# Optimization experiments

Measured on AMD Instinct MI355X. Metric: run time of the kernel, lower is better.

## Reference

```python
import jax, jax.numpy as jnp
import numpy as np

D_MODEL, D_K, D_V = 1024, 64, 64
B, S = 2, 4096
NEG = 1e9


def setup_inputs() -> dict:
    key = jax.random.key(0)
    ks = jax.random.split(key, 10)
    Q = jax.random.normal(ks[0], (B, S, D_MODEL), dtype=jnp.float32)
    K = jax.random.normal(ks[1], (B, S, D_MODEL), dtype=jnp.float32)
    V = jax.random.normal(ks[2], (B, S, D_MODEL), dtype=jnp.float32)
    mask = jax.random.randint(ks[3], (B, S, S), 0, 2, dtype=jnp.int32)
    sc = 1.0 / np.sqrt(D_MODEL)
    Wq = jax.random.normal(ks[4], (D_K, D_MODEL), dtype=jnp.float32) * sc
    bq = jnp.zeros((D_K,), dtype=jnp.float32)
    Wk = jax.random.normal(ks[5], (D_K, D_MODEL), dtype=jnp.float32) * sc
    bk = jnp.zeros((D_K,), dtype=jnp.float32)
    Wv = jax.random.normal(ks[6], (D_V, D_MODEL), dtype=jnp.float32) * sc
    bv = jnp.zeros((D_V,), dtype=jnp.float32)
    return {"Q": Q, "K": K, "V": V, "mask": mask,
            "Wq": Wq, "bq": bq, "Wk": Wk, "bk": bk, "Wv": Wv, "bv": bv}


def reference(Q, K, V, mask, Wq, bq, Wk, bk, Wv, bv):
    # Linear projections: q,k -> [B,S,d_k], v -> [B,S,d_v]
    q = jnp.einsum('bsm,km->bsk', Q, Wq) + bq
    k = jnp.einsum('bsm,km->bsk', K, Wk) + bk
    v = jnp.einsum('bsm,vm->bsv', V, Wv) + bv
    # Scaled dot-product scores [B,S,S]
    x = jnp.einsum('bqk,bsk->bqs', q, k) / jnp.sqrt(jnp.float32(D_K))
    m = mask.astype(x.dtype)
    x = x * m - NEG * (1.0 - m)
    x = jax.nn.softmax(x, axis=2)
    y = jnp.einsum('bqs,bsv->bqv', x, v)
    return y
```

## Files before the change

### kernel.cpp

```cpp
#include <hip/hip_runtime.h>

typedef unsigned short u16;
typedef unsigned long long u64;
typedef __bf16 bf16x8 __attribute__((ext_vector_type(8)));
typedef float f32x4 __attribute__((ext_vector_type(4)));

#define MFMA16(a, b, c) __builtin_amdgcn_mfma_f32_16x16x32_bf16((a), (b), (c), 0, 0, 0)

__device__ __forceinline__ bf16x8 ld8(const u16* p) {
    return *reinterpret_cast<const bf16x8*>(p);
}

__device__ __forceinline__ unsigned pk2(float a, float b) {
    unsigned short ua = __builtin_bit_cast(unsigned short, (__bf16)a);
    unsigned short ub = __builtin_bit_cast(unsigned short, (__bf16)b);
    return (unsigned)ua | ((unsigned)ub << 16);
}

__device__ __forceinline__ bf16x8 cvt8(float4 a, float4 b) {
    bf16x8 r;
    r[0] = (__bf16)a.x; r[1] = (__bf16)a.y; r[2] = (__bf16)a.z; r[3] = (__bf16)a.w;
    r[4] = (__bf16)b.x; r[5] = (__bf16)b.y; r[6] = (__bf16)b.z; r[7] = (__bf16)b.w;
    return r;
}

__global__ __launch_bounds__(256) void packcvt_kernel(
    const int* __restrict__ mask, u64* __restrict__ bits,
    const float* __restrict__ Wq, const float* __restrict__ Wk,
    const float* __restrict__ Wv, u16* __restrict__ wb)
{
    if (blockIdx.x >= 2048) {
        const int t = (blockIdx.x - 2048) * 256 + threadIdx.x;
        const int mat = t >> 13;
        const int idx = (t & 8191) * 8;
        const float* src = (mat == 0) ? Wq : (mat == 1) ? Wk : Wv;
        float4 a = *(const float4*)(src + idx);
        float4 b = *(const float4*)(src + idx + 4);
        uint4 o;
        o.x = pk2(a.x, a.y); o.y = pk2(a.z, a.w);
        o.z = pk2(b.x, b.y); o.w = pk2(b.z, b.w);
        *reinterpret_cast<uint4*>(wb + (size_t)mat * 65536 + idx) = o;
        return;
    }

    const int lane = threadIdx.x & 63, w = threadIdx.x >> 6;
    const int row = blockIdx.x * 4 + w;
    const int* mp = mask + (size_t)row * 4096 + lane * 4;
    u64* op = bits + (size_t)row * 64;

    int4 h0[8], h1[8];
    #pragma unroll
    for (int j = 0; j < 8; ++j) h0[j] = *(const int4*)(mp + j * 256);
    #pragma unroll
    for (int j = 0; j < 8; ++j) h1[j] = *(const int4*)(mp + 2048 + j * 256);

    u64 mine0 = 0, mine1 = 0;
    #pragma unroll
    for (int j = 0; j < 8; ++j) {
        const u64 b0 = __ballot(h0[j].x != 0);
        const u64 b1 = __ballot(h0[j].y != 0);
        const u64 b2 = __ballot(h0[j].z != 0);
        const u64 b3 = __ballot(h0[j].w != 0);
        if (lane == j * 4 + 0) mine0 = b0;
        if (lane == j * 4 + 1) mine0 = b1;
        if (lane == j * 4 + 2) mine0 = b2;
        if (lane == j * 4 + 3) mine0 = b3;
        const u64 c0 = __ballot(h1[j].x != 0);
        const u64 c1 = __ballot(h1[j].y != 0);
        const u64 c2 = __ballot(h1[j].z != 0);
        const u64 c3 = __ballot(h1[j].w != 0);
        if (lane == j * 4 + 0) mine1 = c0;
        if (lane == j * 4 + 1) mine1 = c1;
        if (lane == j * 4 + 2) mine1 = c2;
        if (lane == j * 4 + 3) mine1 = c3;
    }
    if (lane < 32) { op[lane] = mine0; op[32 + lane] = mine1; }
}

__global__ __launch_bounds__(256, 1) void proj_kernel(
    const float* __restrict__ Q, const float* __restrict__ K, const float* __restrict__ V,
    const float* __restrict__ bq, const float* __restrict__ bk, const float* __restrict__ bv,
    const u16* __restrict__ wb, u16* __restrict__ qb, u16* __restrict__ kb,
    u16* __restrict__ vtb)
{
    const int mat  = blockIdx.x >> 7;
    const int tile = blockIdx.x & 127;
    const int lane = threadIdx.x & 63;
    const int w    = threadIdx.x >> 6;
    const int c = lane & 15, g = lane >> 4;

    const float* X = (mat == 0) ? Q : (mat == 1) ? K : V;
    const u16*   W = wb + (size_t)mat * 65536;

    const int rw = tile * 64 + w * 16;
    const float* xp = X + (size_t)(rw + c) * 1024 + g * 8;
    const u16*   wp = W + (size_t)c * 1024 + g * 8;

    f32x4 acc[4] = {};

    float4 A[8], B[8];
    #pragma unroll
    for (int j = 0; j < 8; ++j) {
        A[j] = *(const float4*)(xp + j * 32);
        B[j] = *(const float4*)(xp + j * 32 + 4);
    }

    #pragma unroll 1
    for (int kt = 0; kt < 4; ++kt) {
        const int base  = kt * 8;
        const int nbase = (kt < 3) ? base + 8 : base;
        #pragma unroll
        for (int j = 0; j < 8; ++j) {
            const bf16x8 a = cvt8(A[j], B[j]);
            A[j] = *(const float4*)(xp + (nbase + j) * 32);
            B[j] = *(const float4*)(xp + (nbase + j) * 32 + 4);
            const u16* wk = wp + (base + j) * 32;
            if (mat < 2) {
                #pragma unroll
                for (int t = 0; t < 4; ++t)
                    acc[t] = MFMA16(a, ld8(wk + t * 16384), acc[t]);
            } else {
                #pragma unroll
                for (int t = 0; t < 4; ++t)
                    acc[t] = MFMA16(ld8(wk + t * 16384), a, acc[t]);
            }
        }
    }

    if (mat < 2) {
        const float* bias = (mat == 0) ? bq : bk;
        u16* dst = (mat == 0) ? qb : kb;
        #pragma unroll
        for (int t = 0; t < 4; ++t) {
            const float bz = bias[t * 16 + c];
            #pragma unroll
            for (int r = 0; r < 4; ++r) {
                const int row = rw + g * 4 + r;
                dst[(size_t)row * 64 + t * 16 + c] =
                    __builtin_bit_cast(u16, (__bf16)(acc[t][r] + bz));
            }
        }
    } else {
        const int sg = rw + c;
        const int bidx = sg >> 12, sin = sg & 4095;
        #pragma unroll
        for (int t = 0; t < 4; ++t) {
            #pragma unroll
            for (int r = 0; r < 4; ++r) {
                const int dv = t * 16 + g * 4 + r;
                vtb[(size_t)(bidx * 64 + dv) * 4096 + sin] =
                    __builtin_bit_cast(u16, (__bf16)(acc[t][r] + bv[dv]));
            }
        }
    }
}

__global__ __launch_bounds__(256) void attn_kernel(
    const u64* __restrict__ bits, const u16* __restrict__ qb,
    const u16* __restrict__ kb, const u16* __restrict__ vtb,
    float* __restrict__ pacc, float* __restrict__ pm, float* __restrict__ pl)
{
    __shared__ uint2 plds[4][128];
    const int lane = threadIdx.x & 63, w = threadIdx.x >> 6;
    const int c = lane & 15, g = lane >> 4;
    const int gw    = blockIdx.x * 4 + w;
    const int strip = gw >> 3;
    const int chunk = gw & 7;
    const int b     = strip >> 8;
    const int q0    = (strip & 255) * 16;
    const int sBase = chunk * 512;
    const float SSC = 0.18033688011112042f;

    const u16* qrow = qb + (size_t)((b << 12) + q0 + c) * 64 + g * 8;
    const bf16x8 qf0 = ld8(qrow);
    const bf16x8 qf1 = ld8(qrow + 32);

    const u16* kfp = kb  + (((size_t)b << 12) + sBase + c) * 64 + g * 8;
    const u16* vfp = vtb + (size_t)(b * 64 + c) * 4096 + sBase + g * 8;

    const u64* bp = bits + (size_t)((b << 12) + q0 + c) * 64 + chunk * 8;
    const u64 Wd0 = bp[0], Wd1 = bp[1], Wd2 = bp[2], Wd3 = bp[3];
    const u64 Wd4 = bp[4], Wd5 = bp[5], Wd6 = bp[6], Wd7 = bp[7];

    f32x4 acc0 = {}, acc1 = {}, acc2 = {}, acc3 = {};
    const f32x4 zf = {};
    float m_run = -__builtin_inff(), l_run = 0.f;

    bf16x8 k00 = ld8(kfp),            k01 = ld8(kfp + 32);
    bf16x8 k10 = ld8(kfp + 16 * 64),  k11 = ld8(kfp + 16 * 64 + 32);

    #pragma unroll
    for (int half = 0; half < 2; ++half) {
        const u64 Wr0 = half ? Wd4 : Wd0;
        const u64 Wr1 = half ? Wd5 : Wd1;
        const u64 Wr2 = half ? Wd6 : Wd2;
        const u64 Wr3 = half ? Wd7 : Wd3;
        #pragma unroll 1
        for (int it2 = 0; it2 < 8; ++it2) {
            const int it = half * 8 + it2;
            const int s0 = sBase + it * 32;

            const u16* vp = vfp + it * 32;
            const bf16x8 v0 = ld8(vp);
            const bf16x8 v1 = ld8(vp + 16 * 4096);
            const bf16x8 v2 = ld8(vp + 32 * 4096);
            const bf16x8 v3 = ld8(vp + 48 * 4096);

            f32x4 d0 = MFMA16(k00, qf0, zf);
            d0 = MFMA16(k01, qf1, d0);
            f32x4 d1 = MFMA16(k10, qf0, zf);
            d1 = MFMA16(k11, qf1, d1);

            const int no = (it < 15) ? (it + 1) * 2048 : it * 2048;
            k00 = ld8(kfp + no);            k01 = ld8(kfp + no + 32);
            k10 = ld8(kfp + no + 16 * 64);  k11 = ld8(kfp + no + 16 * 64 + 32);

            const int sh = it2 * 8 + g;
            const unsigned t0 = (unsigned)(Wr0 >> sh);
            const unsigned t1 = (unsigned)(Wr1 >> sh);
            const unsigned t2 = (unsigned)(Wr2 >> sh);
            const unsigned t3 = (unsigned)(Wr3 >> sh);

            const float x0 = (t0 & 1u)  ? d0[0] * SSC : -1e9f;
            const float x1 = (t1 & 1u)  ? d0[1] * SSC : -1e9f;
            const float x2 = (t2 & 1u)  ? d0[2] * SSC : -1e9f;
            const float x3 = (t3 & 1u)  ? d0[3] * SSC : -1e9f;
            const float x4 = (t0 & 16u) ? d1[0] * SSC : -1e9f;
            const float x5 = (t1 & 16u) ? d1[1] * SSC : -1e9f;
            const float x6 = (t2 & 16u) ? d1[2] * SSC : -1e9f;
            const float x7 = (t3 & 16u) ? d1[3] * SSC : -1e9f;

            float tm = fmaxf(fmaxf(fmaxf(x0, x1), fmaxf(x2, x3)),
                             fmaxf(fmaxf(x4, x5), fmaxf(x6, x7)));
            tm = fmaxf(tm, __shfl_xor(tm, 16));
            tm = fmaxf(tm, __shfl_xor(tm, 32));
            const float m_new = fmaxf(m_run, tm);
            const float f = exp2f(m_run - m_new);

            const float p0 = exp2f(x0 - m_new), p1 = exp2f(x1 - m_new);
            const float p2 = exp2f(x2 - m_new), p3 = exp2f(x3 - m_new);
            const float p4 = exp2f(x4 - m_new), p5 = exp2f(x5 - m_new);
            const float p6 = exp2f(x6 - m_new), p7 = exp2f(x7 - m_new);
            float rs = ((p0 + p1) + (p2 + p3)) + ((p4 + p5) + (p6 + p7));
            rs += __shfl_xor(rs, 16);
            rs += __shfl_xor(rs, 32);
            l_run = l_run * f + rs;
            m_run = m_new;

            plds[w][c * 8 + ( g      ^ (c & 7))] = make_uint2(pk2(p0, p1), pk2(p2, p3));
            plds[w][c * 8 + ((g + 4) ^ (c & 7))] = make_uint2(pk2(p4, p5), pk2(p6, p7));

            if (__any(f < 1.0f)) {
                const float f0 = __shfl(f, g * 4 + 0);
                const float f1 = __shfl(f, g * 4 + 1);
                const float f2 = __shfl(f, g * 4 + 2);
                const float f3 = __shfl(f, g * 4 + 3);
                acc0[0] *= f0; acc0[1] *= f1; acc0[2] *= f2; acc0[3] *= f3;
                acc1[0] *= f0; acc1[1] *= f1; acc1[2] *= f2; acc1[3] *= f3;
                acc2[0] *= f0; acc2[1] *= f1; acc2[2] *= f2; acc2[3] *= f3;
                acc3[0] *= f0; acc3[1] *= f1; acc3[2] *= f2; acc3[3] *= f3;
            }

            union { uint2 u[2]; bf16x8 v; } pa;
            pa.u[0] = plds[w][c * 8 + ((2 * g    ) ^ (c & 7))];
            pa.u[1] = plds[w][c * 8 + ((2 * g + 1) ^ (c & 7))];

            acc0 = MFMA16(pa.v, v0, acc0);
            acc1 = MFMA16(pa.v, v1, acc1);
            acc2 = MFMA16(pa.v, v2, acc2);
            acc3 = MFMA16(pa.v, v3, acc3);
        }
    }

    const size_t pidx = (size_t)(strip * 8 + chunk) * 16;
    #pragma unroll
    for (int r = 0; r < 4; ++r) {
        const size_t row = pidx + g * 4 + r;
        pacc[row * 64 +  0 + c] = acc0[r];
        pacc[row * 64 + 16 + c] = acc1[r];
        pacc[row * 64 + 32 + c] = acc2[r];
        pacc[row * 64 + 48 + c] = acc3[r];
    }
    if (lane < 16) {
        pm[pidx + c] = m_run;
        pl[pidx + c] = l_run;
    }
}

__global__ __launch_bounds__(256) void comb_kernel(
    const float* __restrict__ pacc, const float* __restrict__ pm,
    const float* __restrict__ pl, float* __restrict__ out)
{
    const int t = blockIdx.x * 256 + threadIdx.x;
    const int r = t >> 6, dv = t & 63;
    const int strip = r >> 4, qi = r & 15;
    const int base = strip * 128 + qi;
    float mv[8];
    float M = -__builtin_inff();
    #pragma unroll
    for (int cc = 0; cc < 8; ++cc) { mv[cc] = pm[base + cc * 16]; M = fmaxf(M, mv[cc]); }
    float num = 0.f, den = 0.f;
    #pragma unroll
    for (int cc = 0; cc < 8; ++cc) {
        const float wgt = exp2f(mv[cc] - M);
        num += wgt * pacc[(size_t)(base + cc * 16) * 64 + dv];
        den += wgt * pl[base + cc * 16];
    }
    out[t] = num / den;
}

extern "C" void kernel_launch(void* const* d_in, const int* in_sizes, int n_in,
                              void* d_out, int out_size, void* d_ws, size_t ws_size,
                              hipStream_t stream)
{
    const float* Q    = (const float*)d_in[0];
    const float* K    = (const float*)d_in[1];
    const float* V    = (const float*)d_in[2];
    const int*   mask = (const int*)d_in[3];
    const float* Wq   = (const float*)d_in[4];
    const float* bq   = (const float*)d_in[5];
    const float* Wk   = (const float*)d_in[6];
    const float* bk   = (const float*)d_in[7];
    const float* Wv   = (const float*)d_in[8];
    const float* bv   = (const float*)d_in[9];
    float* out = (float*)d_out;

    char* ws = (char*)d_ws;
    u16*   wb   = (u16*)(ws);
    u16*   qb   = (u16*)(ws + 393216);
    u16*   kb   = (u16*)(ws + 393216 + 1048576);
    u16*   vtb  = (u16*)(ws + 393216 + 2097152);
    u64*   bits = (u64*)(ws + 4194304);
    float* pm   = (float*)(ws + 8388608);
    float* pl   = (float*)(ws + 8388608 + 262144);
    float* pacc = (float*)(ws + 8388608 + 524288);

    packcvt_kernel<<<2144, 256, 0, stream>>>(mask, bits, Wq, Wk, Wv, wb);
    proj_kernel<<<384, 256, 0, stream>>>(Q, K, V, bq, bk, bv, wb, qb, kb, vtb);
    attn_kernel<<<1024, 256, 0, stream>>>(bits, qb, kb, vtb, pacc, pm, pl);
    comb_kernel<<<2048, 256, 0, stream>>>(pacc, pm, pl, out);
}
```

Baseline: 145.5 us.

## Fuse mask bit-packing into projection kernel with async LDS-staged loads

Splits weight conversion into its own small kernel and merges the mask-to-bitmask packing with the Q/K/V projection into one launch. Projection blocks and mask blocks now run concurrently, so the bandwidth-bound mask read can overlap the MFMA-bound projection. Both paths stage global data through LDS with global_load_lds in a three-slot ring, with explicit vmcnt waits and an XOR swizzle on the activation tiles. The projection blocks lose the `(256, 1)` launch bound, and the hand-written waitcnt schedule is fragile if the compiler reorders loads.

```diff
diff --git a/kernel.cpp b/kernel.cpp
--- a/kernel.cpp
+++ b/kernel.cpp
@@ -6,6 +6,13 @@
 typedef float f32x4 __attribute__((ext_vector_type(4)));
 
 #define MFMA16(a, b, c) __builtin_amdgcn_mfma_f32_16x16x32_bf16((a), (b), (c), 0, 0, 0)
+#define WAITVM(N) asm volatile("s_waitcnt vmcnt(" #N ")" ::: "memory")
+
+__device__ __forceinline__ void gld16(const void* g, void* l) {
+    __builtin_amdgcn_global_load_lds(
+        (const __attribute__((address_space(1))) void*)g,
+        (__attribute__((address_space(3))) void*)l, 16, 0, 0);
+}
 
 __device__ __forceinline__ bf16x8 ld8(const u16* p) {
     return *reinterpret_cast<const bf16x8*>(p);
@@ -24,107 +31,124 @@
     return r;
 }
 
-__global__ __launch_bounds__(256) void packcvt_kernel(
-    const int* __restrict__ mask, u64* __restrict__ bits,
+__global__ __launch_bounds__(256) void wcvt_kernel(
     const float* __restrict__ Wq, const float* __restrict__ Wk,
     const float* __restrict__ Wv, u16* __restrict__ wb)
 {
-    if (blockIdx.x >= 2048) {
-        const int t = (blockIdx.x - 2048) * 256 + threadIdx.x;
-        const int mat = t >> 13;
-        const int idx = (t & 8191) * 8;
-        const float* src = (mat == 0) ? Wq : (mat == 1) ? Wk : Wv;
-        float4 a = *(const float4*)(src + idx);
-        float4 b = *(const float4*)(src + idx + 4);
-        uint4 o;
-        o.x = pk2(a.x, a.y); o.y = pk2(a.z, a.w);
-        o.z = pk2(b.x, b.y); o.w = pk2(b.z, b.w);
-        *reinterpret_cast<uint4*>(wb + (size_t)mat * 65536 + idx) = o;
-        return;
-    }
-
-    const int lane = threadIdx.x & 63, w = threadIdx.x >> 6;
-    const int row = blockIdx.x * 4 + w;
-    const int* mp = mask + (size_t)row * 4096 + lane * 4;
-    u64* op = bits + (size_t)row * 64;
-
-    int4 h0[8], h1[8];
-    #pragma unroll
-    for (int j = 0; j < 8; ++j) h0[j] = *(const int4*)(mp + j * 256);
-    #pragma unroll
-    for (int j = 0; j < 8; ++j) h1[j] = *(const int4*)(mp + 2048 + j * 256);
-
-    u64 mine0 = 0, mine1 = 0;
-    #pragma unroll
-    for (int j = 0; j < 8; ++j) {
-        const u64 b0 = __ballot(h0[j].x != 0);
-        const u64 b1 = __ballot(h0[j].y != 0);
-        const u64 b2 = __ballot(h0[j].z != 0);
-        const u64 b3 = __ballot(h0[j].w != 0);
-        if (lane == j * 4 + 0) mine0 = b0;
-        if (lane == j * 4 + 1) mine0 = b1;
-        if (lane == j * 4 + 2) mine0 = b2;
-        if (lane == j * 4 + 3) mine0 = b3;
-        const u64 c0 = __ballot(h1[j].x != 0);
-        const u64 c1 = __ballot(h1[j].y != 0);
-        const u64 c2 = __ballot(h1[j].z != 0);
-        const u64 c3 = __ballot(h1[j].w != 0);
-        if (lane == j * 4 + 0) mine1 = c0;
-        if (lane == j * 4 + 1) mine1 = c1;
-        if (lane == j * 4 + 2) mine1 = c2;
-        if (lane == j * 4 + 3) mine1 = c3;
-    }
-    if (lane < 32) { op[lane] = mine0; op[32 + lane] = mine1; }
-}
-
-__global__ __launch_bounds__(256, 1) void proj_kernel(
+    const int t = blockIdx.x * 256 + threadIdx.x;
+    const int mat = t >> 13;
+    const int idx = (t & 8191) * 8;
+    const float* src = (mat == 0) ? Wq : (mat == 1) ? Wk : Wv;
+    float4 a = *(const float4*)(src + idx);
+    float4 b = *(const float4*)(src + idx + 4);
+    uint4 o;
+    o.x = pk2(a.x, a.y); o.y = pk2(a.z, a.w);
+    o.z = pk2(b.x, b.y); o.w = pk2(b.z, b.w);
+    *reinterpret_cast<uint4*>(wb + (size_t)mat * 65536 + idx) = o;
+}
+
+__global__ __launch_bounds__(256) void fused_kernel(
     const float* __restrict__ Q, const float* __restrict__ K, const float* __restrict__ V,
     const float* __restrict__ bq, const float* __restrict__ bk, const float* __restrict__ bv,
-    const u16* __restrict__ wb, u16* __restrict__ qb, u16* __restrict__ kb,
-    u16* __restrict__ vtb)
-{
+    const u16* __restrict__ wb, const int* __restrict__ mask,
+    u16* __restrict__ qb, u16* __restrict__ kb, u16* __restrict__ vtb,
+    u64* __restrict__ bits)
+{
+    __shared__ float ldsf[4][3][512];
+    const int lane = threadIdx.x & 63, w = threadIdx.x >> 6;
+
+    if (blockIdx.x >= 384) {
+        const int gwv = (blockIdx.x - 384) * 4 + w;
+        const int row = gwv >> 1, h = gwv & 1;
+        const int* mp = mask + (size_t)row * 4096 + h * 2048 + lane * 4;
+        int* ldsw = (int*)&ldsf[w][0][0];
+
+        gld16(mp +    0, ldsw +    0);
+        gld16(mp +  256, ldsw +  256);
+        gld16(mp +  512, ldsw +  512);
+        gld16(mp +  768, ldsw +  768);
+
+        u64 mine = 0;
+        #pragma unroll
+        for (int st = 0; st < 4; ++st) {
+            const int slot = st % 3;
+            if (st < 2) {
+                gld16(mp + (st + 2) * 512,       ldsw + ((st + 2) % 3) * 512);
+                gld16(mp + (st + 2) * 512 + 256, ldsw + ((st + 2) % 3) * 512 + 256);
+            }
+            if (st < 2)       { WAITVM(4); }
+            else if (st == 2) { WAITVM(2); }
+            else              { WAITVM(0); }
+            #pragma unroll
+            for (int wdw = 0; wdw < 2; ++wdw) {
+                const int4 m4 = *(const int4*)(ldsw + slot * 512 + wdw * 256 + lane * 4);
+                const u64 b0 = __ballot(m4.x != 0);
+                const u64 b1 = __ballot(m4.y != 0);
+                const u64 b2 = __ballot(m4.z != 0);
+                const u64 b3 = __ballot(m4.w != 0);
+                const int base = (st * 2 + wdw) * 4;
+                if (lane == base + 0) mine = b0;
+                if (lane == base + 1) mine = b1;
+                if (lane == base + 2) mine = b2;
+                if (lane == base + 3) mine = b3;
+            }
+        }
+        if (lane < 32) bits[(size_t)row * 64 + h * 32 + lane] = mine;
+        return;
+    }
+
     const int mat  = blockIdx.x >> 7;
     const int tile = blockIdx.x & 127;
-    const int lane = threadIdx.x & 63;
-    const int w    = threadIdx.x >> 6;
     const int c = lane & 15, g = lane >> 4;
 
     const float* X = (mat == 0) ? Q : (mat == 1) ? K : V;
     const u16*   W = wb + (size_t)mat * 65536;
-
     const int rw = tile * 64 + w * 16;
-    const float* xp = X + (size_t)(rw + c) * 1024 + g * 8;
-    const u16*   wp = W + (size_t)c * 1024 + g * 8;
-
+
+    const int srow = lane >> 3;
+    const int sgr  = (lane & 7) ^ srow;
+    const float* s0p = X + (size_t)(rw + srow) * 1024 + sgr * 4;
+    const float* s1p = s0p + 8 * 1024;
+    float* ldsw = &ldsf[w][0][0];
+
+    const int G1 = c * 8 + ((2 * g)     ^ (c & 7));
+    const int G2 = c * 8 + ((2 * g + 1) ^ (c & 7));
+
+    const u16* wp = W + (size_t)c * 1024 + g * 8;
     f32x4 acc[4] = {};
 
-    float4 A[8], B[8];
-    #pragma unroll
-    for (int j = 0; j < 8; ++j) {
-        A[j] = *(const float4*)(xp + j * 32);
-        B[j] = *(const float4*)(xp + j * 32 + 4);
-    }
-
+    gld16(s0p +  0, ldsw +    0);
+    gld16(s1p +  0, ldsw +  256);
+    gld16(s0p + 32, ldsw +  512);
+    gld16(s1p + 32, ldsw +  768);
+
+    int slot = 0;
     #pragma unroll 1
-    for (int kt = 0; kt < 4; ++kt) {
-        const int base  = kt * 8;
-        const int nbase = (kt < 3) ? base + 8 : base;
-        #pragma unroll
-        for (int j = 0; j < 8; ++j) {
-            const bf16x8 a = cvt8(A[j], B[j]);
-            A[j] = *(const float4*)(xp + (nbase + j) * 32);
-            B[j] = *(const float4*)(xp + (nbase + j) * 32 + 4);
-            const u16* wk = wp + (base + j) * 32;
-            if (mat < 2) {
-                #pragma unroll
-                for (int t = 0; t < 4; ++t)
-                    acc[t] = MFMA16(a, ld8(wk + t * 16384), acc[t]);
-            } else {
-                #pragma unroll
-                for (int t = 0; t < 4; ++t)
-                    acc[t] = MFMA16(ld8(wk + t * 16384), a, acc[t]);
-            }
-        }
+    for (int kk = 0; kk < 32; ++kk) {
+        if (kk < 30) {
+            const int ns = (slot == 0) ? 2 : slot - 1;
+            gld16(s0p + (kk + 2) * 32, ldsw + ns * 512);
+            gld16(s1p + (kk + 2) * 32, ldsw + ns * 512 + 256);
+        }
+        if (kk < 30)       { WAITVM(4); }
+        else if (kk == 30) { WAITVM(2); }
+        else               { WAITVM(0); }
+
+        const float4 xa = *(const float4*)(ldsw + slot * 512 + G1 * 4);
+        const float4 xb = *(const float4*)(ldsw + slot * 512 + G2 * 4);
+        const bf16x8 a = cvt8(xa, xb);
+
+        const u16* wk = wp + kk * 32;
+        if (mat < 2) {
+            #pragma unroll
+            for (int t = 0; t < 4; ++t)
+                acc[t] = MFMA16(a, ld8(wk + t * 16384), acc[t]);
+        } else {
+            #pragma unroll
+            for (int t = 0; t < 4; ++t)
+                acc[t] = MFMA16(ld8(wk + t * 16384), a, acc[t]);
+        }
+        slot = (slot == 2) ? 0 : slot + 1;
     }
 
     if (mat < 2) {
@@ -198,7 +222,6 @@
         #pragma unroll 1
         for (int it2 = 0; it2 < 8; ++it2) {
             const int it = half * 8 + it2;
-            const int s0 = sBase + it * 32;
 
             const u16* vp = vfp + it * 32;
             const bf16x8 v0 = ld8(vp);
@@ -335,8 +358,9 @@
     float* pl   = (float*)(ws + 8388608 + 262144);
     float* pacc = (float*)(ws + 8388608 + 524288);
 
-    packcvt_kernel<<<2144, 256, 0, stream>>>(mask, bits, Wq, Wk, Wv, wb);
-    proj_kernel<<<384, 256, 0, stream>>>(Q, K, V, bq, bk, bv, wb, qb, kb, vtb);
+    wcvt_kernel<<<96, 256, 0, stream>>>(Wq, Wk, Wv, wb);
+    fused_kernel<<<4480, 256, 0, stream>>>(Q, K, V, bq, bk, bv, wb, mask,
+                                           qb, kb, vtb, bits);
     attn_kernel<<<1024, 256, 0, stream>>>(bits, qb, kb, vtb, pacc, pm, pl);
     comb_kernel<<<2048, 256, 0, stream>>>(pacc, pm, pl, out);
 }
```

Measured after the change: 127.1 us. -12.6%, faster.

## Split mask packing into grid-strided kernel and stagger projection K-loop phases

Applied to the files above, without the earlier changes.

The combined pack/convert kernel is split into a small weight-conversion kernel and a separate mask-bit packing kernel. The packing kernel processes 256-int chunks with a grid-strided layout and a 4-deep rolling prefetch, so each wave writes 4 u64 words per chunk rather than buffering 16 loads per row. The projection kernel rotates each wave's K-dimension start by a per-wave phase, which spreads concurrent accesses across different weight and input columns to reduce channel or cache conflicts. It also shortens the prefetch depth from 8 to 4, fully unrolls the loop and drops the occupancy-1 launch bound. The extra launch adds a little overhead, and the reduced prefetch depth may expose more load latency.

```diff
diff --git a/kernel.cpp b/kernel.cpp
--- a/kernel.cpp
+++ b/kernel.cpp
@@ -24,60 +24,54 @@
     return r;
 }
 
-__global__ __launch_bounds__(256) void packcvt_kernel(
-    const int* __restrict__ mask, u64* __restrict__ bits,
+__global__ __launch_bounds__(256) void wcvt_kernel(
     const float* __restrict__ Wq, const float* __restrict__ Wk,
     const float* __restrict__ Wv, u16* __restrict__ wb)
 {
-    if (blockIdx.x >= 2048) {
-        const int t = (blockIdx.x - 2048) * 256 + threadIdx.x;
-        const int mat = t >> 13;
-        const int idx = (t & 8191) * 8;
-        const float* src = (mat == 0) ? Wq : (mat == 1) ? Wk : Wv;
-        float4 a = *(const float4*)(src + idx);
-        float4 b = *(const float4*)(src + idx + 4);
-        uint4 o;
-        o.x = pk2(a.x, a.y); o.y = pk2(a.z, a.w);
-        o.z = pk2(b.x, b.y); o.w = pk2(b.z, b.w);
-        *reinterpret_cast<uint4*>(wb + (size_t)mat * 65536 + idx) = o;
-        return;
-    }
-
-    const int lane = threadIdx.x & 63, w = threadIdx.x >> 6;
-    const int row = blockIdx.x * 4 + w;
-    const int* mp = mask + (size_t)row * 4096 + lane * 4;
-    u64* op = bits + (size_t)row * 64;
-
-    int4 h0[8], h1[8];
-    #pragma unroll
-    for (int j = 0; j < 8; ++j) h0[j] = *(const int4*)(mp + j * 256);
-    #pragma unroll
-    for (int j = 0; j < 8; ++j) h1[j] = *(const int4*)(mp + 2048 + j * 256);
-
-    u64 mine0 = 0, mine1 = 0;
-    #pragma unroll
-    for (int j = 0; j < 8; ++j) {
-        const u64 b0 = __ballot(h0[j].x != 0);
-        const u64 b1 = __ballot(h0[j].y != 0);
-        const u64 b2 = __ballot(h0[j].z != 0);
-        const u64 b3 = __ballot(h0[j].w != 0);
-        if (lane == j * 4 + 0) mine0 = b0;
-        if (lane == j * 4 + 1) mine0 = b1;
-        if (lane == j * 4 + 2) mine0 = b2;
-        if (lane == j * 4 + 3) mine0 = b3;
-        const u64 c0 = __ballot(h1[j].x != 0);
-        const u64 c1 = __ballot(h1[j].y != 0);
-        const u64 c2 = __ballot(h1[j].z != 0);
-        const u64 c3 = __ballot(h1[j].w != 0);
-        if (lane == j * 4 + 0) mine1 = c0;
-        if (lane == j * 4 + 1) mine1 = c1;
-        if (lane == j * 4 + 2) mine1 = c2;
-        if (lane == j * 4 + 3) mine1 = c3;
-    }
-    if (lane < 32) { op[lane] = mine0; op[32 + lane] = mine1; }
-}
-
-__global__ __launch_bounds__(256, 1) void proj_kernel(
+    const int t = blockIdx.x * 256 + threadIdx.x;
+    const int mat = t >> 13;
+    const int idx = (t & 8191) * 8;
+    const float* src = (mat == 0) ? Wq : (mat == 1) ? Wk : Wv;
+    float4 a = *(const float4*)(src + idx);
+    float4 b = *(const float4*)(src + idx + 4);
+    uint4 o;
+    o.x = pk2(a.x, a.y); o.y = pk2(a.z, a.w);
+    o.z = pk2(b.x, b.y); o.w = pk2(b.z, b.w);
+    *reinterpret_cast<uint4*>(wb + (size_t)mat * 65536 + idx) = o;
+}
+
+__global__ __launch_bounds__(256) void pack_kernel(
+    const int* __restrict__ mask, u64* __restrict__ bits)
+{
+    const int lane = threadIdx.x & 63;
+    const int g = (blockIdx.x * 256 + threadIdx.x) >> 6;
+    const int W = gridDim.x * 4;
+
+    int4 h[4];
+    #pragma unroll
+    for (int k = 0; k < 4; ++k)
+        h[k] = *(const int4*)(mask + (size_t)(g + k * W) * 256 + lane * 4);
+
+    #pragma unroll
+    for (int k = 0; k < 16; ++k) {
+        const int4 m4 = h[k & 3];
+        if (k < 12)
+            h[k & 3] = *(const int4*)(mask + (size_t)(g + (k + 4) * W) * 256 + lane * 4);
+
+        const u64 b0 = __ballot(m4.x != 0);
+        const u64 b1 = __ballot(m4.y != 0);
+        const u64 b2 = __ballot(m4.z != 0);
+        const u64 b3 = __ballot(m4.w != 0);
+        u64 myb = b0;
+        if (lane == 1) myb = b1;
+        if (lane == 2) myb = b2;
+        if (lane == 3) myb = b3;
+        const size_t s = (size_t)(g + k * W);
+        if (lane < 4) bits[s * 4 + lane] = myb;
+    }
+}
+
+__global__ __launch_bounds__(256) void proj_kernel(
     const float* __restrict__ Q, const float* __restrict__ K, const float* __restrict__ V,
     const float* __restrict__ bq, const float* __restrict__ bk, const float* __restrict__ bv,
     const u16* __restrict__ wb, u16* __restrict__ qb, u16* __restrict__ kb,
@@ -88,6 +82,7 @@
     const int lane = threadIdx.x & 63;
     const int w    = threadIdx.x >> 6;
     const int c = lane & 15, g = lane >> 4;
+    const int phase = (tile * 4 + w) & 31;
 
     const float* X = (mat == 0) ? Q : (mat == 1) ? K : V;
     const u16*   W = wb + (size_t)mat * 65536;
@@ -98,32 +93,32 @@
 
     f32x4 acc[4] = {};
 
-    float4 A[8], B[8];
-    #pragma unroll
-    for (int j = 0; j < 8; ++j) {
-        A[j] = *(const float4*)(xp + j * 32);
-        B[j] = *(const float4*)(xp + j * 32 + 4);
-    }
-
-    #pragma unroll 1
-    for (int kt = 0; kt < 4; ++kt) {
-        const int base  = kt * 8;
-        const int nbase = (kt < 3) ? base + 8 : base;
-        #pragma unroll
-        for (int j = 0; j < 8; ++j) {
-            const bf16x8 a = cvt8(A[j], B[j]);
-            A[j] = *(const float4*)(xp + (nbase + j) * 32);
-            B[j] = *(const float4*)(xp + (nbase + j) * 32 + 4);
-            const u16* wk = wp + (base + j) * 32;
-            if (mat < 2) {
-                #pragma unroll
-                for (int t = 0; t < 4; ++t)
-                    acc[t] = MFMA16(a, ld8(wk + t * 16384), acc[t]);
-            } else {
-                #pragma unroll
-                for (int t = 0; t < 4; ++t)
-                    acc[t] = MFMA16(ld8(wk + t * 16384), a, acc[t]);
-            }
+    float4 A[4], B[4];
+    #pragma unroll
+    for (int j = 0; j < 4; ++j) {
+        const int kka = (phase + j) & 31;
+        A[j] = *(const float4*)(xp + kka * 32);
+        B[j] = *(const float4*)(xp + kka * 32 + 4);
+    }
+
+    #pragma unroll
+    for (int kk = 0; kk < 32; ++kk) {
+        const int kka = (phase + kk) & 31;
+        const bf16x8 a = cvt8(A[kk & 3], B[kk & 3]);
+        if (kk < 28) {
+            const int kn = (phase + kk + 4) & 31;
+            A[kk & 3] = *(const float4*)(xp + kn * 32);
+            B[kk & 3] = *(const float4*)(xp + kn * 32 + 4);
+        }
+        const u16* wk = wp + kka * 32;
+        if (mat < 2) {
+            #pragma unroll
+            for (int t = 0; t < 4; ++t)
+                acc[t] = MFMA16(a, ld8(wk + t * 16384), acc[t]);
+        } else {
+            #pragma unroll
+            for (int t = 0; t < 4; ++t)
+                acc[t] = MFMA16(ld8(wk + t * 16384), a, acc[t]);
         }
     }
 
@@ -198,7 +193,6 @@
         #pragma unroll 1
         for (int it2 = 0; it2 < 8; ++it2) {
             const int it = half * 8 + it2;
-            const int s0 = sBase + it * 32;
 
             const u16* vp = vfp + it * 32;
             const bf16x8 v0 = ld8(vp);
@@ -335,7 +329,8 @@
     float* pl   = (float*)(ws + 8388608 + 262144);
     float* pacc = (float*)(ws + 8388608 + 524288);
 
-    packcvt_kernel<<<2144, 256, 0, stream>>>(mask, bits, Wq, Wk, Wv, wb);
+    wcvt_kernel<<<96, 256, 0, stream>>>(Wq, Wk, Wv, wb);
+    pack_kernel<<<2048, 256, 0, stream>>>(mask, bits);
     proj_kernel<<<384, 256, 0, stream>>>(Q, K, V, bq, bk, bv, wb, qb, kb, vtb);
     attn_kernel<<<1024, 256, 0, stream>>>(bits, qb, kb, vtb, pacc, pm, pl);
     comb_kernel<<<2048, 256, 0, stream>>>(pacc, pm, pl, out);
```

Measured after the change: 147.8 us. Within noise of the previous version (+1.6%).

## Merge mask bit-packing into projection kernel and use nontemporal streaming loads

Applied to the files above, without the earlier changes.

Splits the weight conversion into its own small kernel and puts the mask bit-packing blocks into the same launch as the Q/K/V projection blocks. Both phases are memory-bound and now run concurrently instead of back-to-back. Mask and activation reads use nontemporal loads to avoid polluting cache. The projection's prefetch depth drops from 8 to 4 and its loop is fully unrolled, which lowers register pressure now that launch_bounds no longer forces one block per SM.

```diff
diff --git a/kernel.cpp b/kernel.cpp
--- a/kernel.cpp
+++ b/kernel.cpp
@@ -4,6 +4,7 @@
 typedef unsigned long long u64;
 typedef __bf16 bf16x8 __attribute__((ext_vector_type(8)));
 typedef float f32x4 __attribute__((ext_vector_type(4)));
+typedef int i32x4 __attribute__((ext_vector_type(4)));
 
 #define MFMA16(a, b, c) __builtin_amdgcn_mfma_f32_16x16x32_bf16((a), (b), (c), 0, 0, 0)
 
@@ -17,76 +18,82 @@
     return (unsigned)ua | ((unsigned)ub << 16);
 }
 
-__device__ __forceinline__ bf16x8 cvt8(float4 a, float4 b) {
+__device__ __forceinline__ bf16x8 cvt8(f32x4 a, f32x4 b) {
     bf16x8 r;
-    r[0] = (__bf16)a.x; r[1] = (__bf16)a.y; r[2] = (__bf16)a.z; r[3] = (__bf16)a.w;
-    r[4] = (__bf16)b.x; r[5] = (__bf16)b.y; r[6] = (__bf16)b.z; r[7] = (__bf16)b.w;
+    r[0] = (__bf16)a[0]; r[1] = (__bf16)a[1]; r[2] = (__bf16)a[2]; r[3] = (__bf16)a[3];
+    r[4] = (__bf16)b[0]; r[5] = (__bf16)b[1]; r[6] = (__bf16)b[2]; r[7] = (__bf16)b[3];
     return r;
 }
 
-__global__ __launch_bounds__(256) void packcvt_kernel(
-    const int* __restrict__ mask, u64* __restrict__ bits,
+__device__ __forceinline__ f32x4 ntf4(const float* p) {
+    return __builtin_nontemporal_load(reinterpret_cast<const f32x4*>(p));
+}
+__device__ __forceinline__ i32x4 nti4(const int* p) {
+    return __builtin_nontemporal_load(reinterpret_cast<const i32x4*>(p));
+}
+
+__global__ __launch_bounds__(256) void wcvt_kernel(
     const float* __restrict__ Wq, const float* __restrict__ Wk,
     const float* __restrict__ Wv, u16* __restrict__ wb)
 {
-    if (blockIdx.x >= 2048) {
-        const int t = (blockIdx.x - 2048) * 256 + threadIdx.x;
-        const int mat = t >> 13;
-        const int idx = (t & 8191) * 8;
-        const float* src = (mat == 0) ? Wq : (mat == 1) ? Wk : Wv;
-        float4 a = *(const float4*)(src + idx);
-        float4 b = *(const float4*)(src + idx + 4);
-        uint4 o;
-        o.x = pk2(a.x, a.y); o.y = pk2(a.z, a.w);
-        o.z = pk2(b.x, b.y); o.w = pk2(b.z, b.w);
-        *reinterpret_cast<uint4*>(wb + (size_t)mat * 65536 + idx) = o;
-        return;
-    }
-
-    const int lane = threadIdx.x & 63, w = threadIdx.x >> 6;
-    const int row = blockIdx.x * 4 + w;
-    const int* mp = mask + (size_t)row * 4096 + lane * 4;
-    u64* op = bits + (size_t)row * 64;
-
-    int4 h0[8], h1[8];
-    #pragma unroll
-    for (int j = 0; j < 8; ++j) h0[j] = *(const int4*)(mp + j * 256);
-    #pragma unroll
-    for (int j = 0; j < 8; ++j) h1[j] = *(const int4*)(mp + 2048 + j * 256);
-
-    u64 mine0 = 0, mine1 = 0;
-    #pragma unroll
-    for (int j = 0; j < 8; ++j) {
-        const u64 b0 = __ballot(h0[j].x != 0);
-        const u64 b1 = __ballot(h0[j].y != 0);
-        const u64 b2 = __ballot(h0[j].z != 0);
-        const u64 b3 = __ballot(h0[j].w != 0);
-        if (lane == j * 4 + 0) mine0 = b0;
-        if (lane == j * 4 + 1) mine0 = b1;
-        if (lane == j * 4 + 2) mine0 = b2;
-        if (lane == j * 4 + 3) mine0 = b3;
-        const u64 c0 = __ballot(h1[j].x != 0);
-        const u64 c1 = __ballot(h1[j].y != 0);
-        const u64 c2 = __ballot(h1[j].z != 0);
-        const u64 c3 = __ballot(h1[j].w != 0);
-        if (lane == j * 4 + 0) mine1 = c0;
-        if (lane == j * 4 + 1) mine1 = c1;
-        if (lane == j * 4 + 2) mine1 = c2;
-        if (lane == j * 4 + 3) mine1 = c3;
-    }
-    if (lane < 32) { op[lane] = mine0; op[32 + lane] = mine1; }
-}
-
-__global__ __launch_bounds__(256, 1) void proj_kernel(
+    const int t = blockIdx.x * 256 + threadIdx.x;
+    const int mat = t >> 13;
+    const int idx = (t & 8191) * 8;
+    const float* src = (mat == 0) ? Wq : (mat == 1) ? Wk : Wv;
+    const f32x4 a = *(const f32x4*)(src + idx);
+    const f32x4 b = *(const f32x4*)(src + idx + 4);
+    uint4 o;
+    o.x = pk2(a[0], a[1]); o.y = pk2(a[2], a[3]);
+    o.z = pk2(b[0], b[1]); o.w = pk2(b[2], b[3]);
+    *reinterpret_cast<uint4*>(wb + (size_t)mat * 65536 + idx) = o;
+}
+
+__global__ __launch_bounds__(256) void fused_kernel(
     const float* __restrict__ Q, const float* __restrict__ K, const float* __restrict__ V,
     const float* __restrict__ bq, const float* __restrict__ bk, const float* __restrict__ bv,
-    const u16* __restrict__ wb, u16* __restrict__ qb, u16* __restrict__ kb,
-    u16* __restrict__ vtb)
-{
+    const u16* __restrict__ wb, const int* __restrict__ mask,
+    u16* __restrict__ qb, u16* __restrict__ kb, u16* __restrict__ vtb,
+    u64* __restrict__ bits)
+{
+    const int lane = threadIdx.x & 63, w = threadIdx.x >> 6;
+
+    if (blockIdx.x >= 384) {
+        const int row = (blockIdx.x - 384) * 4 + w;
+        const int* mp = mask + (size_t)row * 4096 + lane * 4;
+        u64* op = bits + (size_t)row * 64;
+
+        i32x4 h0[8], h1[8];
+        #pragma unroll
+        for (int j = 0; j < 8; ++j) h0[j] = nti4(mp + j * 256);
+        #pragma unroll
+        for (int j = 0; j < 8; ++j) h1[j] = nti4(mp + 2048 + j * 256);
+
+        u64 mine0 = 0, mine1 = 0;
+        #pragma unroll
+        for (int j = 0; j < 8; ++j) {
+            const u64 b0 = __ballot(h0[j][0] != 0);
+            const u64 b1 = __ballot(h0[j][1] != 0);
+            const u64 b2 = __ballot(h0[j][2] != 0);
+            const u64 b3 = __ballot(h0[j][3] != 0);
+            if (lane == j * 4 + 0) mine0 = b0;
+            if (lane == j * 4 + 1) mine0 = b1;
+            if (lane == j * 4 + 2) mine0 = b2;
+            if (lane == j * 4 + 3) mine0 = b3;
+            const u64 c0 = __ballot(h1[j][0] != 0);
+            const u64 c1 = __ballot(h1[j][1] != 0);
+            const u64 c2 = __ballot(h1[j][2] != 0);
+            const u64 c3 = __ballot(h1[j][3] != 0);
+            if (lane == j * 4 + 0) mine1 = c0;
+            if (lane == j * 4 + 1) mine1 = c1;
+            if (lane == j * 4 + 2) mine1 = c2;
+            if (lane == j * 4 + 3) mine1 = c3;
+        }
+        if (lane < 32) { op[lane] = mine0; op[32 + lane] = mine1; }
+        return;
+    }
+
     const int mat  = blockIdx.x >> 7;
     const int tile = blockIdx.x & 127;
-    const int lane = threadIdx.x & 63;
-    const int w    = threadIdx.x >> 6;
     const int c = lane & 15, g = lane >> 4;
 
     const float* X = (mat == 0) ? Q : (mat == 1) ? K : V;
@@ -98,32 +105,29 @@
 
     f32x4 acc[4] = {};
 
-    float4 A[8], B[8];
-    #pragma unroll
-    for (int j = 0; j < 8; ++j) {
-        A[j] = *(const float4*)(xp + j * 32);
-        B[j] = *(const float4*)(xp + j * 32 + 4);
-    }
-
-    #pragma unroll 1
-    for (int kt = 0; kt < 4; ++kt) {
-        const int base  = kt * 8;
-        const int nbase = (kt < 3) ? base + 8 : base;
-        #pragma unroll
-        for (int j = 0; j < 8; ++j) {
-            const bf16x8 a = cvt8(A[j], B[j]);
-            A[j] = *(const float4*)(xp + (nbase + j) * 32);
-            B[j] = *(const float4*)(xp + (nbase + j) * 32 + 4);
-            const u16* wk = wp + (base + j) * 32;
-            if (mat < 2) {
-                #pragma unroll
-                for (int t = 0; t < 4; ++t)
-                    acc[t] = MFMA16(a, ld8(wk + t * 16384), acc[t]);
-            } else {
-                #pragma unroll
-                for (int t = 0; t < 4; ++t)
-                    acc[t] = MFMA16(ld8(wk + t * 16384), a, acc[t]);
-            }
+    f32x4 A[4], B[4];
+    #pragma unroll
+    for (int j = 0; j < 4; ++j) {
+        A[j] = ntf4(xp + j * 32);
+        B[j] = ntf4(xp + j * 32 + 4);
+    }
+
+    #pragma unroll
+    for (int kk = 0; kk < 32; ++kk) {
+        const bf16x8 a = cvt8(A[kk & 3], B[kk & 3]);
+        if (kk < 28) {
+            A[kk & 3] = ntf4(xp + (kk + 4) * 32);
+            B[kk & 3] = ntf4(xp + (kk + 4) * 32 + 4);
+        }
+        const u16* wk = wp + kk * 32;
+        if (mat < 2) {
+            #pragma unroll
+            for (int t = 0; t < 4; ++t)
+                acc[t] = MFMA16(a, ld8(wk + t * 16384), acc[t]);
+        } else {
+            #pragma unroll
+            for (int t = 0; t < 4; ++t)
+                acc[t] = MFMA16(ld8(wk + t * 16384), a, acc[t]);
         }
     }
 
@@ -198,7 +202,6 @@
         #pragma unroll 1
         for (int it2 = 0; it2 < 8; ++it2) {
             const int it = half * 8 + it2;
-            const int s0 = sBase + it * 32;
 
             const u16* vp = vfp + it * 32;
             const bf16x8 v0 = ld8(vp);
@@ -335,8 +338,9 @@
     float* pl   = (float*)(ws + 8388608 + 262144);
     float* pacc = (float*)(ws + 8388608 + 524288);
 
-    packcvt_kernel<<<2144, 256, 0, stream>>>(mask, bits, Wq, Wk, Wv, wb);
-    proj_kernel<<<384, 256, 0, stream>>>(Q, K, V, bq, bk, bv, wb, qb, kb, vtb);
+    wcvt_kernel<<<96, 256, 0, stream>>>(Wq, Wk, Wv, wb);
+    fused_kernel<<<2432, 256, 0, stream>>>(Q, K, V, bq, bk, bv, wb, mask,
+                                           qb, kb, vtb, bits);
     attn_kernel<<<1024, 256, 0, stream>>>(bits, qb, kb, vtb, pacc, pm, pl);
     comb_kernel<<<2048, 256, 0, stream>>>(pacc, pm, pl, out);
 }
```

Measured after the change: 141.5 us. 1.03x faster.
